# Kernel tuning notes

Hardware: AMD Instinct MI355X
Metric: run time of the kernel (lower is better)

## Reference

```python
import jax, jax.numpy as jnp
from jax import lax
import numpy as np


def conv4d(x, w, b, pad):
    """4D conv (stride 1) as a sum of 3D convs over the first-spatial-dim kernel taps.
    x: [B, Cin, T, D, H, W]; w: [Cout, Cin, Kt, Kd, Kh, Kw]; same pad on all dims."""
    B, Cin, T, D, H, W = x.shape
    Cout, _, Kt = w.shape[:3]
    xp = jnp.pad(x, ((0, 0), (0, 0), (pad, pad), (0, 0), (0, 0), (0, 0)))
    Tout = T + 2 * pad - Kt + 1
    acc = None
    for k in range(Kt):  # loop over kernel taps (<=3), not data dims
        xs = xp[:, :, k:k + Tout]                      # [B,Cin,Tout,D,H,W]
        xs = xs.transpose(0, 2, 1, 3, 4, 5).reshape(B * Tout, Cin, D, H, W)
        y = lax.conv_general_dilated(
            xs, w[:, :, k], (1, 1, 1), [(pad, pad)] * 3,
            dimension_numbers=('NCDHW', 'OIDHW', 'NCDHW'))
        acc = y if acc is None else acc + y
    Do, Ho, Wo = acc.shape[2:]
    out = acc.reshape(B, Tout, Cout, Do, Ho, Wo).transpose(0, 2, 1, 3, 4, 5)
    return out + b[None, :, None, None, None, None]


def tconv4d_k2s2(x, w, b):
    """4D transposed conv, kernel=2, stride=2, pad=0 (non-overlapping blocks).
    x: [B,Cin,T,D,H,W]; w: [Cin,Cout,2,2,2,2] (PyTorch ConvTranspose layout)."""
    B, Cin, T, D, H, W = x.shape
    Cout = w.shape[1]
    y = jnp.einsum('bcijkl,copqrs->boipjqkrls', x, w)
    y = y.reshape(B, Cout, 2 * T, 2 * D, 2 * H, 2 * W)
    return y + b[None, :, None, None, None, None]


def setup_inputs() -> dict:
    key = jax.random.key(0)
    ks = jax.random.split(key, 10)
    Cin, Cout = 64, 32
    x1 = jax.random.normal(ks[0], (2, Cin, 8, 8, 8, 8), dtype=jnp.float32)
    x2 = jax.random.normal(ks[1], (2, Cin // 2, 16, 16, 16, 16), dtype=jnp.float32)
    def w(k, shape, fan_in):
        return jax.random.normal(k, shape, dtype=jnp.float32) / np.float32(np.sqrt(fan_in))
    up_w = w(ks[2], (Cin, Cin // 2, 2, 2, 2, 2), Cin * 16)
    up_b = w(ks[3], (Cin // 2,), Cin * 16)
    w1 = w(ks[4], (Cout, Cin, 3, 3, 3, 3), Cin * 81)
    b1 = w(ks[5], (Cout,), Cin * 81)
    w2 = w(ks[6], (Cout, Cout, 3, 3, 3, 3), Cout * 81)
    b2 = w(ks[7], (Cout,), Cout * 81)
    w3 = w(ks[8], (Cout, Cin, 1, 1, 1, 1), Cin)
    b3 = w(ks[9], (Cout,), Cin)
    return {'x1': x1, 'x2': x2, 'up_w': up_w, 'up_b': up_b,
            'w1': w1, 'b1': b1, 'w2': w2, 'b2': b2, 'w3': w3, 'b3': b3}


def reference(x1, x2, up_w, up_b, w1, b1, w2, b2, w3, b3):
    x1u = tconv4d_k2s2(x1, up_w, up_b)              # [B, Cin//2, 16,16,16,16]
    xc = jnp.concatenate([x2, x1u], axis=1)          # [B, Cin, 16,16,16,16]
    Y = jax.nn.relu(conv4d(xc, w1, b1, 1))
    Y = conv4d(Y, w2, b2, 1)
    sc = conv4d(xc, w3, b3, 0)                       # 1x1 residual projection
    return jax.nn.relu(Y + sc)
```

## Files before the change

kernel.cpp:

```cpp
#include <hip/hip_runtime.h>

typedef unsigned short u16;
typedef __attribute__((ext_vector_type(8))) short short8;
typedef __attribute__((ext_vector_type(4))) float f32x4;

#define XCB_OFF  0
#define Y1B_OFF  8388608
#define W1P_OFF  12582912
#define W2P_OFF  12748800
#define W3P_OFF  12831744
#define UPWP_OFF 12833792
#define ZPAD_OFF 12866560

__device__ __forceinline__ u16 f2bf(float v) {
    unsigned u = __builtin_bit_cast(unsigned, v);
    u += 0x7FFFu + ((u >> 16) & 1u);
    return (u16)(u >> 16);
}

__device__ __forceinline__ f32x4 MFMA(short8 a, short8 b, f32x4 c) {
    return __builtin_amdgcn_mfma_f32_16x16x32_bf16(a, b, c, 0, 0, 0);
}

typedef const __attribute__((address_space(1))) u16 gas_u16;
typedef __attribute__((address_space(3))) u16 las_u16;
__device__ __forceinline__ void gload16(const u16* g, u16* l) {
    __builtin_amdgcn_global_load_lds((gas_u16*)g, (las_u16*)l, 16, 0, 0);
}

__global__ __launch_bounds__(256) void setup(const float* __restrict__ w1,
                                             const float* __restrict__ w2,
                                             const float* __restrict__ w3,
                                             const float* __restrict__ upw,
                                             const float* __restrict__ x2,
                                             u16* __restrict__ ws) {
    __shared__ u16 lds[256 * 40];
    int bid = blockIdx.x;
    int tid = threadIdx.x;
    if (bid == 0 && tid < 64) ws[ZPAD_OFF + tid] = 0;

    #pragma unroll
    for (int k = 0; k < 3; ++k) {
        int idx = k * 131072 + bid * 256 + tid;
        if (idx < 165888) {
            int j = idx & 7, lane = (idx >> 3) & 63, rest = idx >> 9;
            int half = rest & 1, chunk = (rest >> 1) & 1, tap = rest >> 2;
            int co = half * 16 + (lane & 15), ci = chunk * 32 + (lane >> 4) * 8 + j;
            ws[W1P_OFF + idx] = f2bf(w1[(co * 64 + ci) * 81 + tap]);
        } else if (idx < 165888 + 82944) {
            int i2 = idx - 165888;
            int j = i2 & 7, lane = (i2 >> 3) & 63, rest = i2 >> 9;
            int half = rest & 1, tap = rest >> 1;
            int co = half * 16 + (lane & 15), ci = (lane >> 4) * 8 + j;
            ws[W2P_OFF + i2] = f2bf(w2[(co * 32 + ci) * 81 + tap]);
        } else if (idx < 165888 + 82944 + 2048) {
            int i3 = idx - (165888 + 82944);
            int j = i3 & 7, lane = (i3 >> 3) & 63, rest = i3 >> 9;
            int half = rest & 1, chunk = rest >> 1;
            int co = half * 16 + (lane & 15), ci = chunk * 32 + (lane >> 4) * 8 + j;
            ws[W3P_OFF + i3] = f2bf(w3[co * 64 + ci]);
        } else if (idx < 250880 + 32768) {
            int i4 = idx - 250880;
            int j = i4 & 7, lane = (i4 >> 3) & 63, rest = i4 >> 9;
            int half = rest & 1, chunk = (rest >> 1) & 1, tap = rest >> 2;
            int co = half * 16 + (lane & 15), ci = chunk * 32 + (lane >> 4) * 8 + j;
            ws[UPWP_OFF + i4] = f2bf(upw[(ci * 32 + co) * 16 + tap]);
        }
    }

    int b = bid >> 8;
    int pos_base = (bid & 255) * 256;
    u16* xcb = ws + XCB_OFF;
    #pragma unroll
    for (int c = 0; c < 32; ++c) {
        lds[tid * 40 + c] = f2bf(x2[((b * 32 + c) << 16) + pos_base + tid]);
    }
    __syncthreads();
    #pragma unroll
    for (int k = 0; k < 4; ++k) {
        int f = k * 256 + tid;
        int u = f & 3, pos = f >> 2;
        uint4 v = *(const uint4*)(lds + pos * 40 + u * 8);
        *(uint4*)(xcb + (size_t)((b << 16) + pos_base + pos) * 64 + u * 8) = v;
    }
}

__global__ __launch_bounds__(256) void xc_up_mfma(const float* __restrict__ x1,
                                                  const u16* __restrict__ upwp,
                                                  const float* __restrict__ up_b,
                                                  u16* __restrict__ xcb) {
    __shared__ u16 lds[64 * 72];
    int tid = threadIdx.x;
    int wv = tid >> 6, lane = tid & 63;
    int q = lane >> 4, m = lane & 15;
    int bid = blockIdx.x;
    int tp = bid & 3, j = (bid >> 2) & 63, b = bid >> 8;
    int pos_base = j * 64;

    #pragma unroll
    for (int g = 0; g < 16; ++g) {
        int c = g * 4 + wv;
        lds[lane * 72 + c] = f2bf(x1[((b * 64 + c) << 12) + pos_base + lane]);
    }
    __syncthreads();

    const short8* wv8 = (const short8*)upwp;
    float4 bi0 = ((const float4*)up_b)[q];
    float4 bi1 = ((const float4*)up_b)[4 + q];
    int it = j >> 3, id = j & 7;

    int tap = tp * 4 + wv;
    f32x4 acc[4][2];
    #pragma unroll
    for (int g = 0; g < 4; ++g) {
        acc[g][0] = (f32x4){bi0.x, bi0.y, bi0.z, bi0.w};
        acc[g][1] = (f32x4){bi1.x, bi1.y, bi1.z, bi1.w};
    }
    #pragma unroll
    for (int chunk = 0; chunk < 2; ++chunk) {
        short8 a0 = wv8[((tap * 2 + chunk) * 2 + 0) * 64 + lane];
        short8 a1 = wv8[((tap * 2 + chunk) * 2 + 1) * 64 + lane];
        #pragma unroll
        for (int g = 0; g < 4; ++g) {
            short8 bf = *(const short8*)(lds + (g * 16 + m) * 72 + chunk * 32 + q * 8);
            acc[g][0] = MFMA(a0, bf, acc[g][0]);
            acc[g][1] = MFMA(a1, bf, acc[g][1]);
        }
    }
    int pt = tap >> 3, pd = (tap >> 2) & 1, ph = (tap >> 1) & 1, pw = tap & 1;
    int oT = 2 * it + pt, oD = 2 * id + pd, oW = 2 * (m & 7) + pw;
    #pragma unroll
    for (int g = 0; g < 4; ++g) {
        int ih = g * 2 + (m >> 3);
        int opos = oT * 4096 + oD * 256 + (2 * ih + ph) * 16 + oW;
        u16* op = xcb + (size_t)((b << 16) + opos) * 64 + 32 + q * 4;
        #pragma unroll
        for (int half = 0; half < 2; ++half) {
            f32x4 v = acc[g][half];
            uint2 o;
            o.x = (unsigned)f2bf(v.x) | ((unsigned)f2bf(v.y) << 16);
            o.y = (unsigned)f2bf(v.z) | ((unsigned)f2bf(v.w) << 16);
            *(uint2*)(op + half * 16) = o;
        }
    }
}

__global__ __launch_bounds__(256, 2) void conv1_mfma(const u16* __restrict__ xcb,
                                                     const u16* __restrict__ w1p,
                                                     const float* __restrict__ b1,
                                                     const u16* __restrict__ zpad,
                                                     u16* __restrict__ y1b) {
    __shared__ __attribute__((aligned(16))) u16 lds[27648];
    int tid = threadIdx.x;
    int lane = tid & 63, wv = tid >> 6;
    int q = lane >> 4, m = lane & 15;
    int c = wv & 1, hf = wv >> 1;
    int bid = blockIdx.x;
    int xcd = bid & 7;
    int b = xcd >> 2, tq = xcd & 3;
    int loc = bid >> 3;
    int hB = loc & 1;
    int d = (loc >> 1) & 15;
    int tl = (loc >> 5) & 3;
    int t = tq * 4 + tl;
    int h0 = hB * 8;
    int rot = (bid * 5) % 9;

    int gofs[6], lofs[6];
    bool st[6], inr[6];
    #pragma unroll
    for (int k = 0; k < 6; ++k) {
        int ui = tid + k * 256;
        int hh = ui / 144, rem = ui - hh * 144;
        int p = rem >> 3, w = rem & 7;
        int u_src = w ^ (p & 7);
        int gh = h0 - 1 + hh, gw = p - 1;
        st[k] = ui < 1440;
        inr[k] = st[k] && ((unsigned)gh < 16u) && ((unsigned)gw < 16u);
        gofs[k] = (gh * 16 + gw) * 64 + u_src * 8;
        lofs[k] = ui * 8;
    }

    f32x4 acc[8];
    if (c == 0) {
        float4 bi = ((const float4*)b1)[hf * 4 + q];
        #pragma unroll
        for (int i = 0; i < 8; ++i)
            acc[i] = (f32x4){bi.x, bi.y, bi.z, bi.w};
    } else {
        #pragma unroll
        for (int i = 0; i < 8; ++i)
            acc[i] = (f32x4){0.f, 0.f, 0.f, 0.f};
    }
    const short8* w1v = (const short8*)w1p;

    auto issue_plane = [&](int ktd, int bb) {
        int kt = ktd / 3, kd = ktd - kt * 3;
        int tt = t + kt - 1, dd = d + kd - 1;
        bool pv = ((unsigned)tt < 16u) && ((unsigned)dd < 16u);
        const u16* src = xcb + (size_t)(((b * 16 + tt) * 16 + dd)) * 16384;
        #pragma unroll
        for (int k = 0; k < 6; ++k) {
            if (st[k]) {
                const u16* g = (pv && inr[k]) ? (src + gofs[k]) : zpad;
                gload16(g, lds + bb * 13824 + lofs[k]);
            }
        }
    };

    issue_plane(rot, 0);
    for (int s = 0; s < 9; ++s) {
        int ktd = rot + s; if (ktd >= 9) ktd -= 9;
        int kt = ktd / 3, kd = ktd - kt * 3;
        __syncthreads();
        short8 W[3][3];
        #pragma unroll
        for (int kw = 0; kw < 3; ++kw)
            #pragma unroll
            for (int kh = 0; kh < 3; ++kh) {
                int tap = ((kt * 3 + kd) * 3 + kh) * 3 + kw;
                W[kw][kh] = w1v[((tap * 2 + c) * 2 + hf) * 64 + lane];
            }
        __builtin_amdgcn_sched_barrier(0);
        if (s < 8) {
            int nk = ktd + 1; if (nk >= 9) nk -= 9;
            issue_plane(nk, (s + 1) & 1);
        }
        __builtin_amdgcn_sched_barrier(0);
        const u16* L = lds + (s & 1) * 13824;
        __builtin_amdgcn_s_setprio(1);
        #pragma unroll
        for (int kw = 0; kw < 3; ++kw) {
            int p = kw + m, pm = p & 7;
            int bo = p * 64 + ((((c << 2) | q) ^ pm) << 3);
            short8 R[10];
            #pragma unroll
            for (int r = 0; r < 10; ++r)
                R[r] = *(const short8*)(L + r * 1152 + bo);
            #pragma unroll
            for (int kh = 0; kh < 3; ++kh) {
                #pragma unroll
                for (int i = 0; i < 8; ++i)
                    acc[i] = MFMA(W[kw][kh], R[i + kh], acc[i]);
            }
        }
        __builtin_amdgcn_s_setprio(0);
    }

    __syncthreads();
    f32x4* buf = (f32x4*)lds;
    if (c == 1) {
        #pragma unroll
        for (int i = 0; i < 8; ++i)
            buf[(hf * 8 + i) * 64 + lane] = acc[i];
    }
    __syncthreads();
    if (c == 0) {
        int obase = ((b * 16 + t) * 16 + d) * 256 + h0 * 16 + m;
        #pragma unroll
        for (int i = 0; i < 8; ++i) {
            int pos = obase + i * 16;
            f32x4 v = acc[i];
            f32x4 w = buf[(hf * 8 + i) * 64 + lane];
            v.x += w.x; v.y += w.y; v.z += w.z; v.w += w.w;
            unsigned r0 = f2bf(fmaxf(v.x, 0.f)), r1 = f2bf(fmaxf(v.y, 0.f));
            unsigned r2 = f2bf(fmaxf(v.z, 0.f)), r3 = f2bf(fmaxf(v.w, 0.f));
            uint2 o;
            o.x = r0 | (r1 << 16);
            o.y = r2 | (r3 << 16);
            *(uint2*)(y1b + (size_t)pos * 32 + hf * 16 + q * 4) = o;
        }
    }
}

__global__ __launch_bounds__(256, 2) void conv2_mfma(const u16* __restrict__ y1b,
                                                     const u16* __restrict__ xcb,
                                                     const u16* __restrict__ w2p,
                                                     const u16* __restrict__ w3p,
                                                     const float* __restrict__ b2,
                                                     const float* __restrict__ b3,
                                                     const u16* __restrict__ zpad,
                                                     float* __restrict__ out) {
    __shared__ __attribute__((aligned(16))) u16 lds[20736];
    int tid = threadIdx.x;
    int lane = tid & 63, wv = tid >> 6;
    int q = lane >> 4, m = lane & 15;
    int hf = wv & 1, rh = wv >> 1;
    int bid = blockIdx.x;
    int xcd = bid & 7;
    int b = xcd >> 2, tq = xcd & 3;
    int loc = bid >> 3;
    int d = loc & 15;
    int tl = (loc >> 4) & 3;
    int t = tq * 4 + tl;
    int rot = (bid * 5) % 9;

    int gofs[6], lofs[6];
    bool st[6], inr[6];
    #pragma unroll
    for (int k = 0; k < 6; ++k) {
        int ui = tid + k * 256;
        int hh = ui / 72, rem = ui - hh * 72;
        int p = rem >> 2, w = rem & 3;
        int u_src = w ^ (p & 3);
        int gh = hh - 1, gw = p - 1;
        st[k] = ui < 1296;
        inr[k] = st[k] && ((unsigned)gh < 16u) && ((unsigned)gw < 16u);
        gofs[k] = (gh * 16 + gw) * 32 + u_src * 8;
        lofs[k] = ui * 8;
    }

    f32x4 acc[8];
    {
        float4 p0 = ((const float4*)b2)[hf * 4 + q];
        float4 s0 = ((const float4*)b3)[hf * 4 + q];
        #pragma unroll
        for (int i = 0; i < 8; ++i)
            acc[i] = (f32x4){p0.x + s0.x, p0.y + s0.y, p0.z + s0.z, p0.w + s0.w};
    }
    const short8* w2v = (const short8*)w2p;

    auto issue_plane = [&](int ktd, int bb) {
        int kt = ktd / 3, kd = ktd - kt * 3;
        int tt = t + kt - 1, dd = d + kd - 1;
        bool pv = ((unsigned)tt < 16u) && ((unsigned)dd < 16u);
        const u16* src = y1b + (size_t)(((b * 16 + tt) * 16 + dd)) * 8192;
        #pragma unroll
        for (int k = 0; k < 6; ++k) {
            if (st[k]) {
                const u16* g = (pv && inr[k]) ? (src + gofs[k]) : zpad;
                gload16(g, lds + bb * 10368 + lofs[k]);
            }
        }
    };

    issue_plane(rot, 0);
    for (int s = 0; s < 9; ++s) {
        int ktd = rot + s; if (ktd >= 9) ktd -= 9;
        __syncthreads();
        short8 W[3][3];
        #pragma unroll
        for (int kw = 0; kw < 3; ++kw)
            #pragma unroll
            for (int kh = 0; kh < 3; ++kh) {
                int tap = (ktd * 3 + kh) * 3 + kw;
                W[kw][kh] = w2v[(tap * 2 + hf) * 64 + lane];
            }
        __builtin_amdgcn_sched_barrier(0);
        if (s < 8) {
            int nk = ktd + 1; if (nk >= 9) nk -= 9;
            issue_plane(nk, (s + 1) & 1);
        }
        __builtin_amdgcn_sched_barrier(0);
        const u16* L = lds + (s & 1) * 10368;
        __builtin_amdgcn_s_setprio(1);
        #pragma unroll
        for (int kw = 0; kw < 3; ++kw) {
            int p = kw + m, pm = p & 3;
            int bo = p * 32 + ((q ^ pm) << 3);
            short8 R[10];
            #pragma unroll
            for (int r = 0; r < 10; ++r)
                R[r] = *(const short8*)(L + (rh * 8 + r) * 576 + bo);
            #pragma unroll
            for (int kh = 0; kh < 3; ++kh) {
                #pragma unroll
                for (int i = 0; i < 8; ++i)
                    acc[i] = MFMA(W[kw][kh], R[i + kh], acc[i]);
            }
        }
        __builtin_amdgcn_s_setprio(0);
    }

    const short8* w3v = (const short8*)w3p;
    int lpos0 = (t * 16 + d) * 256 + (rh * 8) * 16 + m;
    int gpos0 = (b << 16) + lpos0;
    #pragma unroll
    for (int chunk = 0; chunk < 2; ++chunk) {
        short8 a = w3v[(chunk * 2 + hf) * 64 + lane];
        #pragma unroll
        for (int i = 0; i < 8; ++i) {
            short8 bf = *(const short8*)(xcb + (size_t)(gpos0 + i * 16) * 64 + ((chunk << 2) | q) * 8);
            acc[i] = MFMA(a, bf, acc[i]);
        }
    }

    #pragma unroll
    for (int i = 0; i < 8; ++i) {
        int lpos = lpos0 + i * 16;
        f32x4 v = acc[i];
        int co = hf * 16 + q * 4;
        float* op = out + (((size_t)(b * 32 + co)) << 16) + lpos;
        op[0ull << 16] = fmaxf(v.x, 0.f);
        op[1ull << 16] = fmaxf(v.y, 0.f);
        op[2ull << 16] = fmaxf(v.z, 0.f);
        op[3ull << 16] = fmaxf(v.w, 0.f);
    }
}

extern "C" void kernel_launch(void* const* d_in, const int* in_sizes, int n_in,
                              void* d_out, int out_size, void* d_ws, size_t ws_size,
                              hipStream_t stream) {
    const float* x1   = (const float*)d_in[0];
    const float* x2   = (const float*)d_in[1];
    const float* up_w = (const float*)d_in[2];
    const float* up_b = (const float*)d_in[3];
    const float* w1   = (const float*)d_in[4];
    const float* b1   = (const float*)d_in[5];
    const float* w2   = (const float*)d_in[6];
    const float* b2   = (const float*)d_in[7];
    const float* w3   = (const float*)d_in[8];
    const float* b3   = (const float*)d_in[9];
    u16* ws  = (u16*)d_ws;
    float* out = (float*)d_out;

    setup<<<512, 256, 0, stream>>>(w1, w2, w3, up_w, x2, ws);
    xc_up_mfma<<<512, 256, 0, stream>>>(x1, ws + UPWP_OFF, up_b, ws + XCB_OFF);
    conv1_mfma<<<1024, 256, 0, stream>>>(ws + XCB_OFF, ws + W1P_OFF, b1,
                                         ws + ZPAD_OFF, ws + Y1B_OFF);
    conv2_mfma<<<512, 256, 0, stream>>>(ws + Y1B_OFF, ws + XCB_OFF, ws + W2P_OFF,
                                        ws + W3P_OFF, b2, b3, ws + ZPAD_OFF, out);
}
```

Measured before the change: 155.8 us.

## Merge setup and upsample kernels; stage conv2 output through LDS for coalesced stores

After: 158.0 us. Within noise of the previous version (+1.5%).

```diff
diff --git a/kernel.cpp b/kernel.cpp
--- a/kernel.cpp
+++ b/kernel.cpp
@@ -28,119 +28,115 @@
     __builtin_amdgcn_global_load_lds((gas_u16*)g, (las_u16*)l, 16, 0, 0);
 }
 
-__global__ __launch_bounds__(256) void setup(const float* __restrict__ w1,
-                                             const float* __restrict__ w2,
-                                             const float* __restrict__ w3,
-                                             const float* __restrict__ upw,
-                                             const float* __restrict__ x2,
-                                             u16* __restrict__ ws) {
+__global__ __launch_bounds__(256) void pre(const float* __restrict__ w1,
+                                           const float* __restrict__ w2,
+                                           const float* __restrict__ w3,
+                                           const float* __restrict__ upw,
+                                           const float* __restrict__ x1,
+                                           const float* __restrict__ x2,
+                                           const float* __restrict__ up_b,
+                                           u16* __restrict__ ws) {
     __shared__ u16 lds[256 * 40];
     int bid = blockIdx.x;
     int tid = threadIdx.x;
     if (bid == 0 && tid < 64) ws[ZPAD_OFF + tid] = 0;
 
-    #pragma unroll
-    for (int k = 0; k < 3; ++k) {
-        int idx = k * 131072 + bid * 256 + tid;
-        if (idx < 165888) {
-            int j = idx & 7, lane = (idx >> 3) & 63, rest = idx >> 9;
-            int half = rest & 1, chunk = (rest >> 1) & 1, tap = rest >> 2;
-            int co = half * 16 + (lane & 15), ci = chunk * 32 + (lane >> 4) * 8 + j;
-            ws[W1P_OFF + idx] = f2bf(w1[(co * 64 + ci) * 81 + tap]);
-        } else if (idx < 165888 + 82944) {
-            int i2 = idx - 165888;
-            int j = i2 & 7, lane = (i2 >> 3) & 63, rest = i2 >> 9;
-            int half = rest & 1, tap = rest >> 1;
-            int co = half * 16 + (lane & 15), ci = (lane >> 4) * 8 + j;
-            ws[W2P_OFF + i2] = f2bf(w2[(co * 32 + ci) * 81 + tap]);
-        } else if (idx < 165888 + 82944 + 2048) {
-            int i3 = idx - (165888 + 82944);
-            int j = i3 & 7, lane = (i3 >> 3) & 63, rest = i3 >> 9;
-            int half = rest & 1, chunk = rest >> 1;
-            int co = half * 16 + (lane & 15), ci = chunk * 32 + (lane >> 4) * 8 + j;
-            ws[W3P_OFF + i3] = f2bf(w3[co * 64 + ci]);
-        } else if (idx < 250880 + 32768) {
-            int i4 = idx - 250880;
-            int j = i4 & 7, lane = (i4 >> 3) & 63, rest = i4 >> 9;
-            int half = rest & 1, chunk = (rest >> 1) & 1, tap = rest >> 2;
-            int co = half * 16 + (lane & 15), ci = chunk * 32 + (lane >> 4) * 8 + j;
-            ws[UPWP_OFF + i4] = f2bf(upw[(ci * 32 + co) * 16 + tap]);
-        }
-    }
-
-    int b = bid >> 8;
-    int pos_base = (bid & 255) * 256;
-    u16* xcb = ws + XCB_OFF;
-    #pragma unroll
-    for (int c = 0; c < 32; ++c) {
-        lds[tid * 40 + c] = f2bf(x2[((b * 32 + c) << 16) + pos_base + tid]);
-    }
-    __syncthreads();
-    #pragma unroll
-    for (int k = 0; k < 4; ++k) {
-        int f = k * 256 + tid;
-        int u = f & 3, pos = f >> 2;
-        uint4 v = *(const uint4*)(lds + pos * 40 + u * 8);
-        *(uint4*)(xcb + (size_t)((b << 16) + pos_base + pos) * 64 + u * 8) = v;
-    }
-}
-
-__global__ __launch_bounds__(256) void xc_up_mfma(const float* __restrict__ x1,
-                                                  const u16* __restrict__ upwp,
-                                                  const float* __restrict__ up_b,
-                                                  u16* __restrict__ xcb) {
-    __shared__ u16 lds[64 * 72];
-    int tid = threadIdx.x;
-    int wv = tid >> 6, lane = tid & 63;
-    int q = lane >> 4, m = lane & 15;
-    int bid = blockIdx.x;
-    int tp = bid & 3, j = (bid >> 2) & 63, b = bid >> 8;
-    int pos_base = j * 64;
-
-    #pragma unroll
-    for (int g = 0; g < 16; ++g) {
-        int c = g * 4 + wv;
-        lds[lane * 72 + c] = f2bf(x1[((b * 64 + c) << 12) + pos_base + lane]);
-    }
-    __syncthreads();
-
-    const short8* wv8 = (const short8*)upwp;
-    float4 bi0 = ((const float4*)up_b)[q];
-    float4 bi1 = ((const float4*)up_b)[4 + q];
-    int it = j >> 3, id = j & 7;
-
-    int tap = tp * 4 + wv;
-    f32x4 acc[4][2];
-    #pragma unroll
-    for (int g = 0; g < 4; ++g) {
-        acc[g][0] = (f32x4){bi0.x, bi0.y, bi0.z, bi0.w};
-        acc[g][1] = (f32x4){bi1.x, bi1.y, bi1.z, bi1.w};
-    }
-    #pragma unroll
-    for (int chunk = 0; chunk < 2; ++chunk) {
-        short8 a0 = wv8[((tap * 2 + chunk) * 2 + 0) * 64 + lane];
-        short8 a1 = wv8[((tap * 2 + chunk) * 2 + 1) * 64 + lane];
+    if (bid < 512) {
+        #pragma unroll
+        for (int k = 0; k < 3; ++k) {
+            int idx = k * 131072 + bid * 256 + tid;
+            if (idx < 165888) {
+                int j = idx & 7, lane = (idx >> 3) & 63, rest = idx >> 9;
+                int half = rest & 1, chunk = (rest >> 1) & 1, tap = rest >> 2;
+                int co = half * 16 + (lane & 15), ci = chunk * 32 + (lane >> 4) * 8 + j;
+                ws[W1P_OFF + idx] = f2bf(w1[(co * 64 + ci) * 81 + tap]);
+            } else if (idx < 165888 + 82944) {
+                int i2 = idx - 165888;
+                int j = i2 & 7, lane = (i2 >> 3) & 63, rest = i2 >> 9;
+                int half = rest & 1, tap = rest >> 1;
+                int co = half * 16 + (lane & 15), ci = (lane >> 4) * 8 + j;
+                ws[W2P_OFF + i2] = f2bf(w2[(co * 32 + ci) * 81 + tap]);
+            } else if (idx < 165888 + 82944 + 2048) {
+                int i3 = idx - (165888 + 82944);
+                int j = i3 & 7, lane = (i3 >> 3) & 63, rest = i3 >> 9;
+                int half = rest & 1, chunk = rest >> 1;
+                int co = half * 16 + (lane & 15), ci = chunk * 32 + (lane >> 4) * 8 + j;
+                ws[W3P_OFF + i3] = f2bf(w3[co * 64 + ci]);
+            }
+        }
+        int b = bid >> 8;
+        int pos_base = (bid & 255) * 256;
+        u16* xcb = ws + XCB_OFF;
+        #pragma unroll
+        for (int c = 0; c < 32; ++c) {
+            lds[tid * 40 + c] = f2bf(x2[((b * 32 + c) << 16) + pos_base + tid]);
+        }
+        __syncthreads();
+        #pragma unroll
+        for (int k = 0; k < 4; ++k) {
+            int f = k * 256 + tid;
+            int u = f & 3, pos = f >> 2;
+            uint4 v = *(const uint4*)(lds + pos * 40 + u * 8);
+            *(uint4*)(xcb + (size_t)((b << 16) + pos_base + pos) * 64 + u * 8) = v;
+        }
+    } else {
+        int bid2 = bid - 512;
+        int tp = bid2 & 3, j = (bid2 >> 2) & 63, b = bid2 >> 8;
+        int wv = tid >> 6, lane = tid & 63;
+        int q = lane >> 4, m = lane & 15;
+        int pos_base = j * 64;
+        u16* xcb = ws + XCB_OFF;
+
+        #pragma unroll
+        for (int g = 0; g < 16; ++g) {
+            int c = g * 4 + wv;
+            lds[lane * 72 + c] = f2bf(x1[((b * 64 + c) << 12) + pos_base + lane]);
+        }
+        __syncthreads();
+
+        int tap = tp * 4 + wv;
+        float4 bi0 = ((const float4*)up_b)[q];
+        float4 bi1 = ((const float4*)up_b)[4 + q];
+        int it = j >> 3, id = j & 7;
+
+        f32x4 acc[4][2];
         #pragma unroll
         for (int g = 0; g < 4; ++g) {
-            short8 bf = *(const short8*)(lds + (g * 16 + m) * 72 + chunk * 32 + q * 8);
-            acc[g][0] = MFMA(a0, bf, acc[g][0]);
-            acc[g][1] = MFMA(a1, bf, acc[g][1]);
-        }
-    }
-    int pt = tap >> 3, pd = (tap >> 2) & 1, ph = (tap >> 1) & 1, pw = tap & 1;
-    int oT = 2 * it + pt, oD = 2 * id + pd, oW = 2 * (m & 7) + pw;
-    #pragma unroll
-    for (int g = 0; g < 4; ++g) {
-        int ih = g * 2 + (m >> 3);
-        int opos = oT * 4096 + oD * 256 + (2 * ih + ph) * 16 + oW;
-        u16* op = xcb + (size_t)((b << 16) + opos) * 64 + 32 + q * 4;
-        #pragma unroll
-        for (int half = 0; half < 2; ++half) {
-            f32x4 v = acc[g][half];
-            uint2 o;
-            o.x = (unsigned)f2bf(v.x) | ((unsigned)f2bf(v.y) << 16);
-            o.y = (unsigned)f2bf(v.z) | ((unsigned)f2bf(v.w) << 16);
-            *(uint2*)(op + half * 16) = o;
+            acc[g][0] = (f32x4){bi0.x, bi0.y, bi0.z, bi0.w};
+            acc[g][1] = (f32x4){bi1.x, bi1.y, bi1.z, bi1.w};
+        }
+        int co0 = lane & 15, co1 = 16 + (lane & 15);
+        #pragma unroll
+        for (int chunk = 0; chunk < 2; ++chunk) {
+            short8 a0, a1;
+            #pragma unroll
+            for (int jj = 0; jj < 8; ++jj) {
+                int ci = chunk * 32 + (lane >> 4) * 8 + jj;
+                a0[jj] = (short)f2bf(upw[(ci * 32 + co0) * 16 + tap]);
+                a1[jj] = (short)f2bf(upw[(ci * 32 + co1) * 16 + tap]);
+            }
+            #pragma unroll
+            for (int g = 0; g < 4; ++g) {
+                short8 bf = *(const short8*)(lds + (g * 16 + m) * 72 + chunk * 32 + q * 8);
+                acc[g][0] = MFMA(a0, bf, acc[g][0]);
+                acc[g][1] = MFMA(a1, bf, acc[g][1]);
+            }
+        }
+        int pt = tap >> 3, pd = (tap >> 2) & 1, ph = (tap >> 1) & 1, pw = tap & 1;
+        int oT = 2 * it + pt, oD = 2 * id + pd, oW = 2 * (m & 7) + pw;
+        #pragma unroll
+        for (int g = 0; g < 4; ++g) {
+            int ih = g * 2 + (m >> 3);
+            int opos = oT * 4096 + oD * 256 + (2 * ih + ph) * 16 + oW;
+            u16* op = xcb + (size_t)((b << 16) + opos) * 64 + 32 + q * 4;
+            #pragma unroll
+            for (int half = 0; half < 2; ++half) {
+                f32x4 v = acc[g][half];
+                uint2 o;
+                o.x = (unsigned)f2bf(v.x) | ((unsigned)f2bf(v.y) << 16);
+                o.y = (unsigned)f2bf(v.z) | ((unsigned)f2bf(v.w) << 16);
+                *(uint2*)(op + half * 16) = o;
+            }
         }
     }
 }
@@ -281,7 +277,7 @@
                                                      const float* __restrict__ b3,
                                                      const u16* __restrict__ zpad,
                                                      float* __restrict__ out) {
-    __shared__ __attribute__((aligned(16))) u16 lds[20736];
+    __shared__ __attribute__((aligned(16))) u16 lds[33280];
     int tid = threadIdx.x;
     int lane = tid & 63, wv = tid >> 6;
     int q = lane >> 4, m = lane & 15;
@@ -373,7 +369,8 @@
     }
 
     const short8* w3v = (const short8*)w3p;
-    int lpos0 = (t * 16 + d) * 256 + (rh * 8) * 16 + m;
+    int P0 = (t * 16 + d) * 256;
+    int lpos0 = P0 + (rh * 8) * 16 + m;
     int gpos0 = (b << 16) + lpos0;
     #pragma unroll
     for (int chunk = 0; chunk < 2; ++chunk) {
@@ -385,16 +382,23 @@
         }
     }
 
+    __syncthreads();
+    float* lf = (float*)lds;
     #pragma unroll
     for (int i = 0; i < 8; ++i) {
-        int lpos = lpos0 + i * 16;
+        int lp = rh * 128 + i * 16 + m;
         f32x4 v = acc[i];
-        int co = hf * 16 + q * 4;
-        float* op = out + (((size_t)(b * 32 + co)) << 16) + lpos;
-        op[0ull << 16] = fmaxf(v.x, 0.f);
-        op[1ull << 16] = fmaxf(v.y, 0.f);
-        op[2ull << 16] = fmaxf(v.z, 0.f);
-        op[3ull << 16] = fmaxf(v.w, 0.f);
+        lf[(hf * 16 + q * 4 + 0) * 260 + lp] = fmaxf(v.x, 0.f);
+        lf[(hf * 16 + q * 4 + 1) * 260 + lp] = fmaxf(v.y, 0.f);
+        lf[(hf * 16 + q * 4 + 2) * 260 + lp] = fmaxf(v.z, 0.f);
+        lf[(hf * 16 + q * 4 + 3) * 260 + lp] = fmaxf(v.w, 0.f);
+    }
+    __syncthreads();
+    #pragma unroll
+    for (int k = 0; k < 8; ++k) {
+        int co = k * 4 + wv;
+        float4 v = *(const float4*)(lf + co * 260 + lane * 4);
+        *(float4*)(out + (((size_t)(b * 32 + co)) << 16) + P0 + lane * 4) = v;
     }
 }
 
@@ -414,8 +418,7 @@
     u16* ws  = (u16*)d_ws;
     float* out = (float*)d_out;
 
-    setup<<<512, 256, 0, stream>>>(w1, w2, w3, up_w, x2, ws);
-    xc_up_mfma<<<512, 256, 0, stream>>>(x1, ws + UPWP_OFF, up_b, ws + XCB_OFF);
+    pre<<<1024, 256, 0, stream>>>(w1, w2, w3, up_w, x1, x2, up_b, ws);
     conv1_mfma<<<1024, 256, 0, stream>>>(ws + XCB_OFF, ws + W1P_OFF, b1,
                                          ws + ZPAD_OFF, ws + Y1B_OFF);
     conv2_mfma<<<512, 256, 0, stream>>>(ws + Y1B_OFF, ws + XCB_OFF, ws + W2P_OFF,
```

## Drop LDS staging in conv2; load activations directly from global per wave

Applied to the files above, without the earlier changes.

New measurement: 170.2 us. +9.3%, slower.

```diff
diff --git a/kernel.cpp b/kernel.cpp
--- a/kernel.cpp
+++ b/kernel.cpp
@@ -273,7 +273,7 @@
     }
 }
 
-__global__ __launch_bounds__(256, 2) void conv2_mfma(const u16* __restrict__ y1b,
+__global__ __launch_bounds__(256, 4) void conv2_mfma(const u16* __restrict__ y1b,
                                                      const u16* __restrict__ xcb,
                                                      const u16* __restrict__ w2p,
                                                      const u16* __restrict__ w3p,
@@ -281,11 +281,9 @@
                                                      const float* __restrict__ b3,
                                                      const u16* __restrict__ zpad,
                                                      float* __restrict__ out) {
-    __shared__ __attribute__((aligned(16))) u16 lds[20736];
     int tid = threadIdx.x;
-    int lane = tid & 63, wv = tid >> 6;
+    int lane = tid & 63, rg = tid >> 6;
     int q = lane >> 4, m = lane & 15;
-    int hf = wv & 1, rh = wv >> 1;
     int bid = blockIdx.x;
     int xcd = bid & 7;
     int b = xcd >> 2, tq = xcd & 3;
@@ -293,108 +291,84 @@
     int d = loc & 15;
     int tl = (loc >> 4) & 3;
     int t = tq * 4 + tl;
-    int rot = (bid * 5) % 9;
-
-    int gofs[6], lofs[6];
-    bool st[6], inr[6];
-    #pragma unroll
-    for (int k = 0; k < 6; ++k) {
-        int ui = tid + k * 256;
-        int hh = ui / 72, rem = ui - hh * 72;
-        int p = rem >> 2, w = rem & 3;
-        int u_src = w ^ (p & 3);
-        int gh = hh - 1, gw = p - 1;
-        st[k] = ui < 1296;
-        inr[k] = st[k] && ((unsigned)gh < 16u) && ((unsigned)gw < 16u);
-        gofs[k] = (gh * 16 + gw) * 32 + u_src * 8;
-        lofs[k] = ui * 8;
-    }
-
-    f32x4 acc[8];
-    {
+
+    int colofs[3]; bool colok[3];
+    #pragma unroll
+    for (int kw = 0; kw < 3; ++kw) {
+        int gw = kw + m - 1;
+        colok[kw] = (unsigned)gw < 16u;
+        colofs[kw] = gw * 32 + q * 8;
+    }
+
+    f32x4 acc[4][2];
+    #pragma unroll
+    for (int hf = 0; hf < 2; ++hf) {
         float4 p0 = ((const float4*)b2)[hf * 4 + q];
         float4 s0 = ((const float4*)b3)[hf * 4 + q];
         #pragma unroll
-        for (int i = 0; i < 8; ++i)
-            acc[i] = (f32x4){p0.x + s0.x, p0.y + s0.y, p0.z + s0.z, p0.w + s0.w};
+        for (int i = 0; i < 4; ++i)
+            acc[i][hf] = (f32x4){p0.x + s0.x, p0.y + s0.y, p0.z + s0.z, p0.w + s0.w};
     }
     const short8* w2v = (const short8*)w2p;
 
-    auto issue_plane = [&](int ktd, int bb) {
+    #pragma unroll
+    for (int ktd = 0; ktd < 9; ++ktd) {
         int kt = ktd / 3, kd = ktd - kt * 3;
         int tt = t + kt - 1, dd = d + kd - 1;
         bool pv = ((unsigned)tt < 16u) && ((unsigned)dd < 16u);
         const u16* src = y1b + (size_t)(((b * 16 + tt) * 16 + dd)) * 8192;
         #pragma unroll
-        for (int k = 0; k < 6; ++k) {
-            if (st[k]) {
-                const u16* g = (pv && inr[k]) ? (src + gofs[k]) : zpad;
-                gload16(g, lds + bb * 10368 + lofs[k]);
-            }
-        }
-    };
-
-    issue_plane(rot, 0);
-    for (int s = 0; s < 9; ++s) {
-        int ktd = rot + s; if (ktd >= 9) ktd -= 9;
-        __syncthreads();
-        short8 W[3][3];
-        #pragma unroll
-        for (int kw = 0; kw < 3; ++kw)
+        for (int kw = 0; kw < 3; ++kw) {
+            short8 R[6];
+            #pragma unroll
+            for (int r = 0; r < 6; ++r) {
+                int gh = rg * 4 + r - 1;
+                bool ok = pv && colok[kw] && ((unsigned)gh < 16u);
+                const u16* g = ok ? (src + gh * 512 + colofs[kw]) : zpad;
+                R[r] = *(const short8*)g;
+            }
             #pragma unroll
             for (int kh = 0; kh < 3; ++kh) {
                 int tap = (ktd * 3 + kh) * 3 + kw;
-                W[kw][kh] = w2v[(tap * 2 + hf) * 64 + lane];
-            }
-        __builtin_amdgcn_sched_barrier(0);
-        if (s < 8) {
-            int nk = ktd + 1; if (nk >= 9) nk -= 9;
-            issue_plane(nk, (s + 1) & 1);
-        }
-        __builtin_amdgcn_sched_barrier(0);
-        const u16* L = lds + (s & 1) * 10368;
-        __builtin_amdgcn_s_setprio(1);
-        #pragma unroll
-        for (int kw = 0; kw < 3; ++kw) {
-            int p = kw + m, pm = p & 3;
-            int bo = p * 32 + ((q ^ pm) << 3);
-            short8 R[10];
-            #pragma unroll
-            for (int r = 0; r < 10; ++r)
-                R[r] = *(const short8*)(L + (rh * 8 + r) * 576 + bo);
-            #pragma unroll
-            for (int kh = 0; kh < 3; ++kh) {
+                short8 a0 = w2v[(tap * 2 + 0) * 64 + lane];
+                short8 a1 = w2v[(tap * 2 + 1) * 64 + lane];
                 #pragma unroll
-                for (int i = 0; i < 8; ++i)
-                    acc[i] = MFMA(W[kw][kh], R[i + kh], acc[i]);
-            }
-        }
-        __builtin_amdgcn_s_setprio(0);
+                for (int i = 0; i < 4; ++i) {
+                    acc[i][0] = MFMA(a0, R[i + kh], acc[i][0]);
+                    acc[i][1] = MFMA(a1, R[i + kh], acc[i][1]);
+                }
+            }
+        }
     }
 
     const short8* w3v = (const short8*)w3p;
-    int lpos0 = (t * 16 + d) * 256 + (rh * 8) * 16 + m;
+    int lpos0 = (t * 16 + d) * 256 + (rg * 4) * 16 + m;
     int gpos0 = (b << 16) + lpos0;
     #pragma unroll
     for (int chunk = 0; chunk < 2; ++chunk) {
-        short8 a = w3v[(chunk * 2 + hf) * 64 + lane];
-        #pragma unroll
-        for (int i = 0; i < 8; ++i) {
+        short8 a0 = w3v[(chunk * 2 + 0) * 64 + lane];
+        short8 a1 = w3v[(chunk * 2 + 1) * 64 + lane];
+        #pragma unroll
+        for (int i = 0; i < 4; ++i) {
             short8 bf = *(const short8*)(xcb + (size_t)(gpos0 + i * 16) * 64 + ((chunk << 2) | q) * 8);
-            acc[i] = MFMA(a, bf, acc[i]);
-        }
-    }
-
-    #pragma unroll
-    for (int i = 0; i < 8; ++i) {
+            acc[i][0] = MFMA(a0, bf, acc[i][0]);
+            acc[i][1] = MFMA(a1, bf, acc[i][1]);
+        }
+    }
+
+    #pragma unroll
+    for (int i = 0; i < 4; ++i) {
         int lpos = lpos0 + i * 16;
-        f32x4 v = acc[i];
-        int co = hf * 16 + q * 4;
-        float* op = out + (((size_t)(b * 32 + co)) << 16) + lpos;
-        op[0ull << 16] = fmaxf(v.x, 0.f);
-        op[1ull << 16] = fmaxf(v.y, 0.f);
-        op[2ull << 16] = fmaxf(v.z, 0.f);
-        op[3ull << 16] = fmaxf(v.w, 0.f);
+        #pragma unroll
+        for (int hf = 0; hf < 2; ++hf) {
+            f32x4 v = acc[i][hf];
+            int co = hf * 16 + q * 4;
+            float* op = out + (((size_t)(b * 32 + co)) << 16) + lpos;
+            op[0ull << 16] = fmaxf(v.x, 0.f);
+            op[1ull << 16] = fmaxf(v.y, 0.f);
+            op[2ull << 16] = fmaxf(v.z, 0.f);
+            op[3ull << 16] = fmaxf(v.w, 0.f);
+        }
     }
 }
 
```
